# Performance work log

Hardware: AMD Instinct MI355X
Metric: run time of the kernel (lower is better)

The kernel has to match this reference:

```python
import jax, jax.numpy as jnp
import numpy as np

N = 50000      # nodes
E = 800000     # edges
F = 128        # feat_dim
N_RBF = 20
CUTOFF = 5.0


def setup_inputs() -> dict:
    key = jax.random.key(0)
    ks = jax.random.split(key, 10)
    s_j = jax.random.normal(ks[0], (N, F), dtype=jnp.float32)
    v_j = jax.random.normal(ks[1], (N, F, 3), dtype=jnp.float32)
    r_ij = jax.random.normal(ks[2], (E, 3), dtype=jnp.float32)
    nbrs = jax.random.randint(ks[3], (E, 2), 0, N, dtype=jnp.int64)
    # inv_dense: Dense(F->F, swish) then Dense(F->2F)
    W1 = jax.random.normal(ks[4], (F, F), dtype=jnp.float32) / np.sqrt(F)
    b1 = jnp.zeros((F,), dtype=jnp.float32)
    W2 = jax.random.normal(ks[5], (F, 2 * F), dtype=jnp.float32) / np.sqrt(F)
    b2 = jnp.zeros((2 * F,), dtype=jnp.float32)
    # dist_embed: PainnRadialBasis(n_rbf) -> Dense(n_rbf -> 2F), cosine envelope
    Wd = jax.random.normal(ks[6], (N_RBF, 2 * F), dtype=jnp.float32) / np.sqrt(N_RBF)
    bd = jnp.zeros((2 * F,), dtype=jnp.float32)
    return {"s_j": s_j, "v_j": v_j, "r_ij": r_ij, "nbrs": nbrs,
            "W1": W1, "b1": b1, "W2": W2, "b2": b2, "Wd": Wd, "bd": bd}


def reference(s_j, v_j, r_ij, nbrs, W1, b1, W2, b2, Wd, bd):
    # preprocess_r
    dist = jnp.sqrt(jnp.sum(r_ij ** 2 + 1e-8, axis=-1))        # [E]
    unit = r_ij / dist[:, None]                                 # [E,3]

    # InvariantMessage: per-node MLP then gather sender features
    h = jax.nn.silu(s_j @ W1 + b1)                              # [N,F]
    phi_all = h @ W2 + b2                                       # [N,2F]
    phi = phi_all[nbrs[:, 1]]                                   # [E,2F]

    # DistanceEmbed: PaiNN radial basis sin(n*pi*d/cutoff)/d -> Dense -> cosine envelope
    n = jnp.arange(1, N_RBF + 1, dtype=dist.dtype)              # [n_rbf]
    rbf = jnp.sin(n[None, :] * jnp.pi * dist[:, None] / CUTOFF) / dist[:, None]  # [E,n_rbf]
    w_s = rbf @ Wd + bd                                         # [E,2F]
    env = jnp.where(dist < CUTOFF, 0.5 * (jnp.cos(jnp.pi * dist / CUTOFF) + 1.0), 0.0)
    w_s = w_s * env[:, None]

    inv_out = (phi * w_s).reshape(E, 2, F)                      # [E,2,F]
    equi_filter = inv_out[:, 0, :][:, :, None]                  # [E,F,1]
    inv_filter = inv_out[:, 1, :]                               # [E,F]

    delta_v_ij = equi_filter * unit[:, None, :]                 # [E,F,3]
    dest = nbrs[:, 0]
    delta_v_i = jax.ops.segment_sum(delta_v_ij, dest, num_segments=N)  # [N,F,3]
    delta_s_i = jax.ops.segment_sum(inv_filter, dest, num_segments=N)  # [N,F]
    return delta_s_i, delta_v_i
```

## Files before the change

kernel.cpp:

```cpp
#include <hip/hip_runtime.h>
#include <hip/hip_bf16.h>
#include <cstdint>
#include <cstddef>

#define N_NODES 50000
#define N_EDGES 800000
#define FDIM    128
#define NRBF    20
#define CUTOFF_R 5.0f
#define PI_F 3.14159265358979323846f

__global__ void detect_kernel(const int* __restrict__ n32, int* __restrict__ flag)
{
    __shared__ int any;
    if (threadIdx.x == 0) any = 0;
    __syncthreads();
    int nz = 0;
    for (int k = threadIdx.x; k < 1024; k += 256)
        nz |= (n32[2 * k + 1] != 0) ? 1 : 0;
    if (nz) atomicOr(&any, 1);
    __syncthreads();
    if (threadIdx.x == 0) flag[0] = any ? 0 : 1;
}

__global__ __launch_bounds__(256) void node_mlp_kernel(
    const float* __restrict__ S,  const float* __restrict__ W1, const float* __restrict__ b1,
    const float* __restrict__ W2, const float* __restrict__ b2, float* __restrict__ PHI)
{
    __shared__ float sS[64][132];
    __shared__ float sW[4096];

    const int tid  = threadIdx.x;
    const int row0 = blockIdx.x * 64;
    const int ty   = tid >> 4;
    const int tx   = tid & 15;

    for (int i = tid; i < 2048; i += 256) {
        const int r  = i >> 5;
        const int c4 = (i & 31) * 4;
        int gr = row0 + r; if (gr >= N_NODES) gr = N_NODES - 1;
        *reinterpret_cast<float4*>(&sS[r][c4]) =
            *reinterpret_cast<const float4*>(&S[(size_t)gr * FDIM + c4]);
    }

    float acc1[4][8];
    #pragma unroll
    for (int i = 0; i < 4; ++i)
        #pragma unroll
        for (int j = 0; j < 8; ++j) acc1[i][j] = 0.f;

    for (int kk = 0; kk < 128; kk += 32) {
        __syncthreads();
        for (int i = tid; i < 1024; i += 256) {
            const int r  = i >> 5;
            const int c4 = (i & 31) * 4;
            *reinterpret_cast<float4*>(&sW[r * 128 + c4]) =
                *reinterpret_cast<const float4*>(&W1[(size_t)(kk + r) * 128 + c4]);
        }
        __syncthreads();
        #pragma unroll
        for (int k2 = 0; k2 < 32; ++k2) {
            float a[4];
            #pragma unroll
            for (int i = 0; i < 4; ++i) a[i] = sS[ty * 4 + i][kk + k2];
            const float4 b0 = *reinterpret_cast<const float4*>(&sW[k2 * 128 + tx * 4]);
            const float4 b4 = *reinterpret_cast<const float4*>(&sW[k2 * 128 + 64 + tx * 4]);
            const float bb[8] = {b0.x, b0.y, b0.z, b0.w, b4.x, b4.y, b4.z, b4.w};
            #pragma unroll
            for (int i = 0; i < 4; ++i)
                #pragma unroll
                for (int j = 0; j < 8; ++j) acc1[i][j] = fmaf(a[i], bb[j], acc1[i][j]);
        }
    }
    {
        const float4 c0 = *reinterpret_cast<const float4*>(&b1[tx * 4]);
        const float4 c4 = *reinterpret_cast<const float4*>(&b1[64 + tx * 4]);
        const float bb[8] = {c0.x, c0.y, c0.z, c0.w, c4.x, c4.y, c4.z, c4.w};
        #pragma unroll
        for (int i = 0; i < 4; ++i) {
            #pragma unroll
            for (int j = 0; j < 8; ++j) {
                const int c = (j < 4) ? (tx * 4 + j) : (64 + tx * 4 + (j - 4));
                const float x = acc1[i][j] + bb[j];
                sS[ty * 4 + i][c] = x / (1.f + __expf(-x));
            }
        }
    }

    float acc2[4][16];
    #pragma unroll
    for (int i = 0; i < 4; ++i)
        #pragma unroll
        for (int j = 0; j < 16; ++j) acc2[i][j] = 0.f;

    for (int kk = 0; kk < 128; kk += 16) {
        __syncthreads();
        for (int i = tid; i < 1024; i += 256) {
            const int r  = i >> 6;
            const int c4 = (i & 63) * 4;
            *reinterpret_cast<float4*>(&sW[r * 256 + c4]) =
                *reinterpret_cast<const float4*>(&W2[(size_t)(kk + r) * 256 + c4]);
        }
        __syncthreads();
        #pragma unroll
        for (int k2 = 0; k2 < 16; ++k2) {
            float a[4];
            #pragma unroll
            for (int i = 0; i < 4; ++i) a[i] = sS[ty * 4 + i][kk + k2];
            #pragma unroll
            for (int h = 0; h < 4; ++h) {
                const float4 b = *reinterpret_cast<const float4*>(&sW[k2 * 256 + h * 64 + tx * 4]);
                const float bb[4] = {b.x, b.y, b.z, b.w};
                #pragma unroll
                for (int i = 0; i < 4; ++i)
                    #pragma unroll
                    for (int j = 0; j < 4; ++j)
                        acc2[i][h * 4 + j] = fmaf(a[i], bb[j], acc2[i][h * 4 + j]);
            }
        }
    }
    #pragma unroll
    for (int i = 0; i < 4; ++i) {
        const int gr = row0 + ty * 4 + i;
        if (gr < N_NODES) {
            #pragma unroll
            for (int h = 0; h < 4; ++h) {
                const float4 c = *reinterpret_cast<const float4*>(&b2[h * 64 + tx * 4]);
                float4 o;
                o.x = acc2[i][h * 4 + 0] + c.x;
                o.y = acc2[i][h * 4 + 1] + c.y;
                o.z = acc2[i][h * 4 + 2] + c.z;
                o.w = acc2[i][h * 4 + 3] + c.w;
                *reinterpret_cast<float4*>(&PHI[(size_t)gr * 256 + h * 64 + tx * 4]) = o;
            }
        }
    }
}

__global__ void hist_kernel(const int* __restrict__ n32, const int* __restrict__ flag,
                            int* __restrict__ counts)
{
    const int e = blockIdx.x * blockDim.x + threadIdx.x;
    const int str = flag[0] ? 4 : 2;
    if (e < N_EDGES) {
        const int d = n32[(size_t)str * e];
        atomicAdd(&counts[d], 1);
    }
}

__global__ __launch_bounds__(1024) void scan_kernel(const int* __restrict__ counts,
                                                    int* __restrict__ offsets,
                                                    int* __restrict__ cursor)
{
    __shared__ int wsum[16];
    const int t    = threadIdx.x;
    const int lane = t & 63;
    const int wid  = t >> 6;
    const int per  = (N_NODES + 1023) / 1024;
    const int lo   = t * per;
    const int hi   = (lo + per < N_NODES) ? lo + per : N_NODES;

    int s = 0;
    for (int i = lo; i < hi; ++i) s += counts[i];

    int inc = s;
    #pragma unroll
    for (int off = 1; off < 64; off <<= 1) {
        const int v = __shfl_up(inc, off, 64);
        if (lane >= off) inc += v;
    }
    if (lane == 63) wsum[wid] = inc;
    __syncthreads();
    if (t == 0) {
        int run = 0;
        #pragma unroll
        for (int i = 0; i < 16; ++i) { const int v = wsum[i]; wsum[i] = run; run += v; }
        offsets[N_NODES] = run;
    }
    __syncthreads();

    int run = wsum[wid] + inc - s;
    for (int i = lo; i < hi; ++i) {
        offsets[i] = run;
        cursor[i]  = run;
        run += counts[i];
    }
}

__global__ void scatter_kernel(const int* __restrict__ n32, const int* __restrict__ flag,
                               int* __restrict__ cursor, int* __restrict__ csr)
{
    const int e = blockIdx.x * blockDim.x + threadIdx.x;
    const int str = flag[0] ? 4 : 2;
    if (e < N_EDGES) {
        const int d   = n32[(size_t)str * e];
        const int pos = atomicAdd(&cursor[d], 1);
        csr[pos] = e;
    }
}

__global__ __launch_bounds__(256) void gather_kernel(
    const float* __restrict__ PHI, const float* __restrict__ r_ij,
    const int* __restrict__ n32, const int* __restrict__ flag,
    const float* __restrict__ Wd, const float* __restrict__ bd,
    const int* __restrict__ offsets, const int* __restrict__ csr,
    float* __restrict__ out_s, float* __restrict__ out_v)
{
    const int tid  = threadIdx.x;
    const int node = blockIdx.x * 4 + (tid >> 6);
    const int l    = tid & 63;
    if (node >= N_NODES) return;

    float wd0[NRBF], wd1[NRBF], wd2[NRBF], wd3[NRBF];
    #pragma unroll
    for (int n = 0; n < NRBF; ++n) {
        wd0[n] = Wd[n * 256 + l      ];
        wd1[n] = Wd[n * 256 + l + 64 ];
        wd2[n] = Wd[n * 256 + l + 128];
        wd3[n] = Wd[n * 256 + l + 192];
    }
    #pragma unroll
    for (int n = 0; n < NRBF; ++n) {
        asm volatile("" : "+v"(wd0[n]), "+v"(wd1[n]), "+v"(wd2[n]), "+v"(wd3[n]));
    }
    const float bd0 = bd[l], bd1 = bd[l + 64], bd2 = bd[l + 128], bd3 = bd[l + 192];

    const int f64  = flag[0];
    const int str  = f64 ? 4 : 2;
    const int soff = f64 ? 2 : 1;

    const int beg = offsets[node];
    const int end = offsets[node + 1];

    float as0 = 0.f, as1 = 0.f;
    float av0x = 0.f, av0y = 0.f, av0z = 0.f;
    float av1x = 0.f, av1y = 0.f, av1z = 0.f;

    if (beg < end) {
        int e = __builtin_amdgcn_readfirstlane(csr[beg]);
        int j = __builtin_amdgcn_readfirstlane(n32[(size_t)str * e + soff]);
        const float* ph = PHI + (size_t)j * 256;
        float p0 = ph[l], p1 = ph[l + 64], p2 = ph[l + 128], p3 = ph[l + 192];
        float rx = r_ij[3 * (size_t)e + 0];
        float ry = r_ij[3 * (size_t)e + 1];
        float rz = r_ij[3 * (size_t)e + 2];

        for (int p = beg; p < end; ++p) {
            const int pn = (p + 1 < end) ? (p + 1) : p;
            const int e2 = __builtin_amdgcn_readfirstlane(csr[pn]);
            const int j2 = __builtin_amdgcn_readfirstlane(n32[(size_t)str * e2 + soff]);
            const float* ph2 = PHI + (size_t)j2 * 256;
            const float q0 = ph2[l], q1 = ph2[l + 64], q2 = ph2[l + 128], q3 = ph2[l + 192];
            const float sx = r_ij[3 * (size_t)e2 + 0];
            const float sy = r_ij[3 * (size_t)e2 + 1];
            const float sz = r_ij[3 * (size_t)e2 + 2];

            const float d2    = fmaf(rx, rx, fmaf(ry, ry, fmaf(rz, rz, 3e-8f)));
            const float inv_d = __frsqrt_rn(d2);
            const float dist  = d2 * inv_d;
            const float x  = (PI_F / CUTOFF_R) * dist;
            const float sn = __sinf(x);
            const float cn = __cosf(x);
            const float env  = (dist < CUTOFF_R) ? (0.5f * (cn + 1.0f)) : 0.0f;
            const float twoc = cn + cn;

            float w0 = bd0, w1 = bd1, w2 = bd2, w3 = bd3;
            float sm1 = 0.f, scur = sn;
            #pragma unroll
            for (int n = 0; n < NRBF; ++n) {
                const float rb = scur * inv_d;
                w0 = fmaf(rb, wd0[n], w0);
                w1 = fmaf(rb, wd1[n], w1);
                w2 = fmaf(rb, wd2[n], w2);
                w3 = fmaf(rb, wd3[n], w3);
                const float nxt = fmaf(twoc, scur, -sm1);
                sm1 = scur; scur = nxt;
            }

            const float ux = rx * inv_d, uy = ry * inv_d, uz = rz * inv_d;
            const float e0 = p0 * (w0 * env);
            const float e1 = p1 * (w1 * env);
            as0 = fmaf(p2, w2 * env, as0);
            as1 = fmaf(p3, w3 * env, as1);
            av0x = fmaf(e0, ux, av0x); av0y = fmaf(e0, uy, av0y); av0z = fmaf(e0, uz, av0z);
            av1x = fmaf(e1, ux, av1x); av1y = fmaf(e1, uy, av1y); av1z = fmaf(e1, uz, av1z);

            p0 = q0; p1 = q1; p2 = q2; p3 = q3;
            rx = sx; ry = sy; rz = sz;
        }
    }

    out_s[(size_t)node * FDIM + l]      = as0;
    out_s[(size_t)node * FDIM + 64 + l] = as1;
    const size_t vb0 = ((size_t)node * FDIM + l) * 3;
    const size_t vb1 = ((size_t)node * FDIM + 64 + l) * 3;
    out_v[vb0 + 0] = av0x; out_v[vb0 + 1] = av0y; out_v[vb0 + 2] = av0z;
    out_v[vb1 + 0] = av1x; out_v[vb1 + 1] = av1y; out_v[vb1 + 2] = av1z;
}

extern "C" void kernel_launch(void* const* d_in, const int* in_sizes, int n_in,
                              void* d_out, int out_size, void* d_ws, size_t ws_size,
                              hipStream_t stream)
{
    (void)in_sizes; (void)n_in; (void)out_size; (void)ws_size;
    const float* s_j  = (const float*)d_in[0];
    const float* r_ij = (const float*)d_in[2];
    const int*   n32  = (const int*)d_in[3];
    const float* W1   = (const float*)d_in[4];
    const float* b1   = (const float*)d_in[5];
    const float* W2   = (const float*)d_in[6];
    const float* b2   = (const float*)d_in[7];
    const float* Wd   = (const float*)d_in[8];
    const float* bd   = (const float*)d_in[9];

    float* out_s = (float*)d_out;
    float* out_v = out_s + (size_t)N_NODES * FDIM;

    char*  ws      = (char*)d_ws;
    float* PHI     = (float*)(ws);
    int*   counts  = (int*)(ws + 51200000);
    int*   offsets = (int*)(ws + 51400000);
    int*   cursor  = (int*)(ws + 51600128);
    int*   csr     = (int*)(ws + 51800128);
    int*   flag    = (int*)(ws + 55000128);

    hipMemsetAsync(counts, 0, N_NODES * sizeof(int), stream);

    detect_kernel <<<1, 256, 0, stream>>>(n32, flag);
    node_mlp_kernel<<<(N_NODES + 63) / 64, 256, 0, stream>>>(s_j, W1, b1, W2, b2, PHI);
    hist_kernel   <<<(N_EDGES + 255) / 256, 256, 0, stream>>>(n32, flag, counts);
    scan_kernel   <<<1, 1024, 0, stream>>>(counts, offsets, cursor);
    scatter_kernel<<<(N_EDGES + 255) / 256, 256, 0, stream>>>(n32, flag, cursor, csr);
    gather_kernel <<<(N_NODES + 3) / 4, 256, 0, stream>>>(PHI, r_ij, n32, flag, Wd, bd,
                                                          offsets, csr, out_s, out_v);
}
```

Before: 676.5 us.

## Enlarge node MLP tile to 128 rows with 8x8 register blocking

Measured after the change: 711.9 us. 1.05x slower.

```diff
diff --git a/kernel.cpp b/kernel.cpp
--- a/kernel.cpp
+++ b/kernel.cpp
@@ -9,6 +9,7 @@
 #define NRBF    20
 #define CUTOFF_R 5.0f
 #define PI_F 3.14159265358979323846f
+#define SPAD 133
 
 __global__ void detect_kernel(const int* __restrict__ n32, int* __restrict__ flag)
 {
@@ -27,49 +28,53 @@
     const float* __restrict__ S,  const float* __restrict__ W1, const float* __restrict__ b1,
     const float* __restrict__ W2, const float* __restrict__ b2, float* __restrict__ PHI)
 {
-    __shared__ float sS[64][132];
-    __shared__ float sW[4096];
+    __shared__ float sS[128 * SPAD];
+    __shared__ float sW[2048];
 
     const int tid  = threadIdx.x;
-    const int row0 = blockIdx.x * 64;
+    const int row0 = blockIdx.x * 128;
     const int ty   = tid >> 4;
     const int tx   = tid & 15;
 
-    for (int i = tid; i < 2048; i += 256) {
-        const int r  = i >> 5;
-        const int c4 = (i & 31) * 4;
+    #pragma unroll
+    for (int i = 0; i < 16; ++i) {
+        const int idx = tid + i * 256;
+        const int r   = idx >> 5;
+        const int c4  = (idx & 31) * 4;
         int gr = row0 + r; if (gr >= N_NODES) gr = N_NODES - 1;
-        *reinterpret_cast<float4*>(&sS[r][c4]) =
-            *reinterpret_cast<const float4*>(&S[(size_t)gr * FDIM + c4]);
-    }
-
-    float acc1[4][8];
-    #pragma unroll
-    for (int i = 0; i < 4; ++i)
-        #pragma unroll
-        for (int j = 0; j < 8; ++j) acc1[i][j] = 0.f;
-
-    for (int kk = 0; kk < 128; kk += 32) {
+        const float4 v = *reinterpret_cast<const float4*>(&S[(size_t)gr * FDIM + c4]);
+        float* dst = &sS[r * SPAD + c4];
+        dst[0] = v.x; dst[1] = v.y; dst[2] = v.z; dst[3] = v.w;
+    }
+
+    float acc[8][8];
+    #pragma unroll
+    for (int i = 0; i < 8; ++i)
+        #pragma unroll
+        for (int j = 0; j < 8; ++j) acc[i][j] = 0.f;
+
+    for (int kk = 0; kk < 128; kk += 16) {
         __syncthreads();
-        for (int i = tid; i < 1024; i += 256) {
-            const int r  = i >> 5;
-            const int c4 = (i & 31) * 4;
+        #pragma unroll
+        for (int i = 0; i < 2; ++i) {
+            const int idx = tid + i * 256;
+            const int r = idx >> 5, c4 = (idx & 31) * 4;
             *reinterpret_cast<float4*>(&sW[r * 128 + c4]) =
                 *reinterpret_cast<const float4*>(&W1[(size_t)(kk + r) * 128 + c4]);
         }
         __syncthreads();
         #pragma unroll
-        for (int k2 = 0; k2 < 32; ++k2) {
-            float a[4];
-            #pragma unroll
-            for (int i = 0; i < 4; ++i) a[i] = sS[ty * 4 + i][kk + k2];
+        for (int k2 = 0; k2 < 16; ++k2) {
+            float a[8];
+            #pragma unroll
+            for (int i = 0; i < 8; ++i) a[i] = sS[(ty * 8 + i) * SPAD + kk + k2];
             const float4 b0 = *reinterpret_cast<const float4*>(&sW[k2 * 128 + tx * 4]);
             const float4 b4 = *reinterpret_cast<const float4*>(&sW[k2 * 128 + 64 + tx * 4]);
             const float bb[8] = {b0.x, b0.y, b0.z, b0.w, b4.x, b4.y, b4.z, b4.w};
             #pragma unroll
-            for (int i = 0; i < 4; ++i)
+            for (int i = 0; i < 8; ++i)
                 #pragma unroll
-                for (int j = 0; j < 8; ++j) acc1[i][j] = fmaf(a[i], bb[j], acc1[i][j]);
+                for (int j = 0; j < 8; ++j) acc[i][j] = fmaf(a[i], bb[j], acc[i][j]);
         }
     }
     {
@@ -77,61 +82,58 @@
         const float4 c4 = *reinterpret_cast<const float4*>(&b1[64 + tx * 4]);
         const float bb[8] = {c0.x, c0.y, c0.z, c0.w, c4.x, c4.y, c4.z, c4.w};
         #pragma unroll
-        for (int i = 0; i < 4; ++i) {
+        for (int i = 0; i < 8; ++i) {
             #pragma unroll
             for (int j = 0; j < 8; ++j) {
                 const int c = (j < 4) ? (tx * 4 + j) : (64 + tx * 4 + (j - 4));
-                const float x = acc1[i][j] + bb[j];
-                sS[ty * 4 + i][c] = x / (1.f + __expf(-x));
-            }
-        }
-    }
-
-    float acc2[4][16];
-    #pragma unroll
-    for (int i = 0; i < 4; ++i)
-        #pragma unroll
-        for (int j = 0; j < 16; ++j) acc2[i][j] = 0.f;
-
-    for (int kk = 0; kk < 128; kk += 16) {
-        __syncthreads();
-        for (int i = tid; i < 1024; i += 256) {
-            const int r  = i >> 6;
-            const int c4 = (i & 63) * 4;
-            *reinterpret_cast<float4*>(&sW[r * 256 + c4]) =
-                *reinterpret_cast<const float4*>(&W2[(size_t)(kk + r) * 256 + c4]);
-        }
-        __syncthreads();
-        #pragma unroll
-        for (int k2 = 0; k2 < 16; ++k2) {
-            float a[4];
-            #pragma unroll
-            for (int i = 0; i < 4; ++i) a[i] = sS[ty * 4 + i][kk + k2];
-            #pragma unroll
-            for (int h = 0; h < 4; ++h) {
-                const float4 b = *reinterpret_cast<const float4*>(&sW[k2 * 256 + h * 64 + tx * 4]);
-                const float bb[4] = {b.x, b.y, b.z, b.w};
+                const float x = acc[i][j] + bb[j];
+                sS[(ty * 8 + i) * SPAD + c] = x / (1.f + __expf(-x));
+            }
+        }
+    }
+
+    for (int half = 0; half < 2; ++half) {
+        float acc2[8][8];
+        #pragma unroll
+        for (int i = 0; i < 8; ++i)
+            #pragma unroll
+            for (int j = 0; j < 8; ++j) acc2[i][j] = 0.f;
+
+        for (int kk = 0; kk < 128; kk += 8) {
+            __syncthreads();
+            {
+                const int r = tid >> 5, c4 = (tid & 31) * 4;
+                *reinterpret_cast<float4*>(&sW[r * 128 + c4]) =
+                    *reinterpret_cast<const float4*>(&W2[(size_t)(kk + r) * 256 + half * 128 + c4]);
+            }
+            __syncthreads();
+            #pragma unroll
+            for (int k2 = 0; k2 < 8; ++k2) {
+                float a[8];
                 #pragma unroll
-                for (int i = 0; i < 4; ++i)
+                for (int i = 0; i < 8; ++i) a[i] = sS[(ty * 8 + i) * SPAD + kk + k2];
+                const float4 b0 = *reinterpret_cast<const float4*>(&sW[k2 * 128 + tx * 4]);
+                const float4 b4 = *reinterpret_cast<const float4*>(&sW[k2 * 128 + 64 + tx * 4]);
+                const float bb[8] = {b0.x, b0.y, b0.z, b0.w, b4.x, b4.y, b4.z, b4.w};
+                #pragma unroll
+                for (int i = 0; i < 8; ++i)
                     #pragma unroll
-                    for (int j = 0; j < 4; ++j)
-                        acc2[i][h * 4 + j] = fmaf(a[i], bb[j], acc2[i][h * 4 + j]);
-            }
-        }
-    }
-    #pragma unroll
-    for (int i = 0; i < 4; ++i) {
-        const int gr = row0 + ty * 4 + i;
-        if (gr < N_NODES) {
-            #pragma unroll
-            for (int h = 0; h < 4; ++h) {
-                const float4 c = *reinterpret_cast<const float4*>(&b2[h * 64 + tx * 4]);
-                float4 o;
-                o.x = acc2[i][h * 4 + 0] + c.x;
-                o.y = acc2[i][h * 4 + 1] + c.y;
-                o.z = acc2[i][h * 4 + 2] + c.z;
-                o.w = acc2[i][h * 4 + 3] + c.w;
-                *reinterpret_cast<float4*>(&PHI[(size_t)gr * 256 + h * 64 + tx * 4]) = o;
+                    for (int j = 0; j < 8; ++j) acc2[i][j] = fmaf(a[i], bb[j], acc2[i][j]);
+            }
+        }
+        const float4 c0 = *reinterpret_cast<const float4*>(&b2[half * 128 + tx * 4]);
+        const float4 c4 = *reinterpret_cast<const float4*>(&b2[half * 128 + 64 + tx * 4]);
+        #pragma unroll
+        for (int i = 0; i < 8; ++i) {
+            const int gr = row0 + ty * 8 + i;
+            if (gr < N_NODES) {
+                float4 o0, o4;
+                o0.x = acc2[i][0] + c0.x; o0.y = acc2[i][1] + c0.y;
+                o0.z = acc2[i][2] + c0.z; o0.w = acc2[i][3] + c0.w;
+                o4.x = acc2[i][4] + c4.x; o4.y = acc2[i][5] + c4.y;
+                o4.z = acc2[i][6] + c4.z; o4.w = acc2[i][7] + c4.w;
+                *reinterpret_cast<float4*>(&PHI[(size_t)gr * 256 + half * 128 + tx * 4]) = o0;
+                *reinterpret_cast<float4*>(&PHI[(size_t)gr * 256 + half * 128 + 64 + tx * 4]) = o4;
             }
         }
     }
@@ -199,7 +201,7 @@
     }
 }
 
-__global__ __launch_bounds__(256) void gather_kernel(
+__global__ __launch_bounds__(256, 3) void gather_kernel(
     const float* __restrict__ PHI, const float* __restrict__ r_ij,
     const int* __restrict__ n32, const int* __restrict__ flag,
     const float* __restrict__ Wd, const float* __restrict__ bd,
@@ -327,7 +329,7 @@
     hipMemsetAsync(counts, 0, N_NODES * sizeof(int), stream);
 
     detect_kernel <<<1, 256, 0, stream>>>(n32, flag);
-    node_mlp_kernel<<<(N_NODES + 63) / 64, 256, 0, stream>>>(s_j, W1, b1, W2, b2, PHI);
+    node_mlp_kernel<<<(N_NODES + 127) / 128, 256, 0, stream>>>(s_j, W1, b1, W2, b2, PHI);
     hist_kernel   <<<(N_EDGES + 255) / 256, 256, 0, stream>>>(n32, flag, counts);
     scan_kernel   <<<1, 1024, 0, stream>>>(counts, offsets, cursor);
     scatter_kernel<<<(N_EDGES + 255) / 256, 256, 0, stream>>>(n32, flag, cursor, csr);
```
